# Optimization experiments

Measured on AMD Instinct MI355X. Metric: run time of the kernel, lower is better.

Reference implementation:

```python
import jax, jax.numpy as jnp
import numpy as np

N_HEADS = 16
HEAD_DIM = 64
ROPE_BASE = 10000.0


def _rope_cos_sin(T, d, dtype):
    # GPT-NeoX style: inv_freq over even indices, cos/sin duplicated to full head_dim
    inv_freq = 1.0 / (ROPE_BASE ** (jnp.arange(0, d, 2, dtype=jnp.float32) / d))
    freqs = jnp.arange(T, dtype=jnp.float32)[:, None] * inv_freq[None, :]  # [T, d/2]
    emb = jnp.concatenate([freqs, freqs], axis=-1)  # [T, d]
    return jnp.cos(emb).astype(dtype), jnp.sin(emb).astype(dtype)


def _rotate_half(x):
    x1, x2 = jnp.split(x, 2, axis=-1)
    return jnp.concatenate([-x2, x1], axis=-1)


def setup_inputs() -> dict:
    key = jax.random.key(0)
    k1, k2, k3 = jax.random.split(key, 3)
    B, T, C = 2, 2048, 1024
    x = jax.random.normal(k1, (B, T, C), dtype=jnp.float32)
    Wqkv = jax.random.normal(k2, (C, 3 * C), dtype=jnp.float32) * (1.0 / np.sqrt(C))
    Wout = jax.random.normal(k3, (C, C), dtype=jnp.float32) * (1.0 / np.sqrt(C))
    return {"x": x, "Wqkv": Wqkv, "Wout": Wout}


def reference(x, Wqkv, Wout):
    B, T, C = x.shape
    H, D = N_HEADS, HEAD_DIM
    qkv = (x @ Wqkv).reshape(B, T, 3, H, D)
    q, k, v = qkv[:, :, 0], qkv[:, :, 1], qkv[:, :, 2]  # [B,T,H,D]
    q = q.transpose(0, 2, 1, 3)  # [B,H,T,D]
    k = k.transpose(0, 2, 1, 3)
    v = v.transpose(0, 2, 1, 3)
    cos, sin = _rope_cos_sin(T, D, x.dtype)  # [T,D]
    cos = cos[None, None]
    sin = sin[None, None]
    q = q * cos + _rotate_half(q) * sin
    k = k * cos + _rotate_half(k) * sin
    scale = 1.0 / np.sqrt(D)
    scores = jnp.einsum("bhqd,bhkd->bhqk", q, k) * scale  # [B,H,T,T]
    causal = jnp.tril(jnp.ones((T, T), dtype=bool))
    scores = jnp.where(causal[None, None], scores, jnp.finfo(scores.dtype).min)
    attn = jax.nn.softmax(scores, axis=-1)
    out = jnp.einsum("bhqk,bhkd->bhqd", attn, v)  # [B,H,T,D]
    out = out.transpose(0, 2, 1, 3).reshape(B, T, C)
    return out @ Wout
```

## Files before the change

kernel.cpp:

```cpp
#include <hip/hip_runtime.h>


#define B_  2
#define T_  2048
#define C_  1024
#define H_  16
#define D_  64
#define N3_ 3072

typedef unsigned short ushortx8 __attribute__((ext_vector_type(8)));
typedef unsigned short ushortx4 __attribute__((ext_vector_type(4)));
typedef short bf16x8 __attribute__((ext_vector_type(8)));
typedef float f32x4 __attribute__((ext_vector_type(4)));
typedef float f32x16 __attribute__((ext_vector_type(16)));
typedef unsigned int uintx2 __attribute__((ext_vector_type(2)));

__device__ __forceinline__ unsigned short f2bf(float f) {
  union { float f; unsigned u; } v; v.f = f;
  unsigned r = v.u + 0x7FFFu + ((v.u >> 16) & 1u);
  return (unsigned short)(r >> 16);
}
__device__ __forceinline__ float bf2f(unsigned short h) {
  union { unsigned u; float f; } v; v.u = ((unsigned)h) << 16;
  return v.f;
}
__device__ __forceinline__ unsigned cvtpk_bf16(float lo, float hi) {
  unsigned r; asm("v_cvt_pk_bf16_f32 %0, %1, %2" : "=v"(r) : "v"(lo), "v"(hi));
  return r;
}
__device__ __forceinline__ void gload_lds16(const void* g, void* l) {
  __builtin_amdgcn_global_load_lds((const __attribute__((address_space(1))) void*)g,
                                   (__attribute__((address_space(3))) void*)l,
                                   16, 0, 0);
}

__global__ __launch_bounds__(256) void prep_kernel(const float* __restrict__ x,
                                                   unsigned short* __restrict__ Xb,
                                                   const float* __restrict__ Wqkv,
                                                   unsigned short* __restrict__ WqkvT,
                                                   const float* __restrict__ Wout,
                                                   unsigned short* __restrict__ WoutT) {
  __shared__ float tile[32][33];
  const int bid = blockIdx.x;
  if (bid < 4096) {
    size_t i = ((size_t)bid * 256 + threadIdx.x) * 4;
    const float4 v = *(const float4*)(x + i);
    ushortx4 o;
    o[0] = f2bf(v.x); o[1] = f2bf(v.y); o[2] = f2bf(v.z); o[3] = f2bf(v.w);
    *(ushortx4*)(Xb + i) = o;
    return;
  }
  const float* W;
  unsigned short* WT;
  int K, N, n0, k0;
  if (bid < 7168) {
    const int idx = bid - 4096;
    W = Wqkv; WT = WqkvT; K = C_; N = N3_;
    n0 = (idx % (N3_ / 32)) * 32; k0 = (idx / (N3_ / 32)) * 32;
  } else {
    const int idx = bid - 7168;
    W = Wout; WT = WoutT; K = C_; N = C_;
    n0 = (idx % (C_ / 32)) * 32; k0 = (idx / (C_ / 32)) * 32;
  }
  const int tx = threadIdx.x & 31, ty = threadIdx.x >> 5;
#pragma unroll
  for (int i = 0; i < 4; ++i)
    tile[ty + i * 8][tx] = W[(size_t)(k0 + ty + i * 8) * N + n0 + tx];
  __syncthreads();
#pragma unroll
  for (int i = 0; i < 4; ++i)
    WT[(size_t)(n0 + ty + i * 8) * K + k0 + tx] = f2bf(tile[tx][ty + i * 8]);
}

template <int OUTF32>
__global__ __launch_bounds__(256) void gemm_bt_kernel(const unsigned short* __restrict__ A,
                                                      const unsigned short* __restrict__ BT,
                                                      void* __restrict__ Cptr,
                                                      int M, int N, int K) {
  __shared__ unsigned short Alds[128 * 64];
  __shared__ unsigned short Blds[128 * 64];
  const int tid = threadIdx.x;
  const int w = tid >> 6, l = tid & 63;
  const int wr = w >> 1, wc = w & 1;
  const int lg = l >> 4, lr = l & 15;
  const int m0 = blockIdx.y * 128, n0 = blockIdx.x * 128;
  const int lr8 = l >> 3;
  const int lc8 = (l & 7) ^ lr8;

  f32x4 acc[4][4];
#pragma unroll
  for (int i = 0; i < 4; ++i)
#pragma unroll
    for (int j = 0; j < 4; ++j) acc[i][j] = f32x4{0.f, 0.f, 0.f, 0.f};

  for (int k0 = 0; k0 < K; k0 += 64) {
    __syncthreads();
#pragma unroll
    for (int i = 0; i < 4; ++i) {
      const int ch = w * 4 + i;
      gload_lds16(A + (size_t)(m0 + ch * 8 + lr8) * K + k0 + lc8 * 8, &Alds[ch * 512]);
      gload_lds16(BT + (size_t)(n0 + ch * 8 + lr8) * K + k0 + lc8 * 8, &Blds[ch * 512]);
    }
    __syncthreads();
#pragma unroll
    for (int kc = 0; kc < 2; ++kc) {
      bf16x8 af[4], bfr[4];
#pragma unroll
      for (int mi = 0; mi < 4; ++mi) {
        const int row = wr * 64 + mi * 16 + lr;
        const int c16 = (kc * 4 + lg) ^ (row & 7);
        af[mi] = *(const bf16x8*)(&Alds[row * 64 + c16 * 8]);
      }
#pragma unroll
      for (int nj = 0; nj < 4; ++nj) {
        const int row = wc * 64 + nj * 16 + lr;
        const int c16 = (kc * 4 + lg) ^ (row & 7);
        bfr[nj] = *(const bf16x8*)(&Blds[row * 64 + c16 * 8]);
      }
#pragma unroll
      for (int mi = 0; mi < 4; ++mi)
#pragma unroll
        for (int nj = 0; nj < 4; ++nj)
          acc[mi][nj] = __builtin_amdgcn_mfma_f32_16x16x32_bf16(af[mi], bfr[nj], acc[mi][nj], 0, 0, 0);
    }
  }
#pragma unroll
  for (int mi = 0; mi < 4; ++mi)
#pragma unroll
    for (int nj = 0; nj < 4; ++nj)
#pragma unroll
      for (int j = 0; j < 4; ++j) {
        const int row = m0 + wr * 64 + mi * 16 + lg * 4 + j;
        const int col = n0 + wc * 64 + nj * 16 + lr;
        if (OUTF32) ((float*)Cptr)[(size_t)row * N + col] = acc[mi][nj][j];
        else ((unsigned short*)Cptr)[(size_t)row * N + col] = f2bf(acc[mi][nj][j]);
      }
}

__global__ __launch_bounds__(256) void rope_vtrans_kernel(const unsigned short* __restrict__ QKV,
                                                          unsigned short* __restrict__ Qp,
                                                          unsigned short* __restrict__ Kp,
                                                          unsigned short* __restrict__ Vt) {
  __shared__ unsigned short tile[64][72];
  const int tt = blockIdx.x, bh = blockIdx.y;
  const int b = bh >> 4, h = bh & 15;
  const int tid = threadIdx.x;
  if (blockIdx.z == 0) {
    const int half = tid >> 7;
    const int r = (tid >> 1) & 63;
    const int d0 = (tid & 1) * 16;
    const int t = tt * 64 + r;
    const unsigned short* src = QKV + (size_t)(b * T_ + t) * N3_ + half * C_ + h * D_;
    ushortx8 lo0 = *(const ushortx8*)(src + d0);
    ushortx8 lo1 = *(const ushortx8*)(src + d0 + 8);
    ushortx8 hi0 = *(const ushortx8*)(src + d0 + 32);
    ushortx8 hi1 = *(const ushortx8*)(src + d0 + 40);
    ushortx8 olo0, olo1, ohi0, ohi1;
    const float scale = half ? 1.0f : 0.18033688011112042f;
    const float tf = (float)t;
#pragma unroll
    for (int jj = 0; jj < 16; ++jj) {
      const int d = d0 + jj;
      const float invf = exp2f((float)d * -0.41524101186092036f);
      const float ang = tf * invf;
      const float c = cosf(ang), s = sinf(ang);
      const float xl = bf2f(jj < 8 ? lo0[jj] : lo1[jj - 8]);
      const float xh = bf2f(jj < 8 ? hi0[jj] : hi1[jj - 8]);
      const unsigned short rl = f2bf((xl * c - xh * s) * scale);
      const unsigned short rh = f2bf((xh * c + xl * s) * scale);
      if (jj < 8) { olo0[jj] = rl; ohi0[jj] = rh; }
      else        { olo1[jj - 8] = rl; ohi1[jj - 8] = rh; }
    }
    unsigned short* dst = (half ? Kp : Qp) + ((size_t)bh * T_ + t) * D_;
    *(ushortx8*)(dst + d0) = olo0;
    *(ushortx8*)(dst + d0 + 8) = olo1;
    *(ushortx8*)(dst + d0 + 32) = ohi0;
    *(ushortx8*)(dst + d0 + 40) = ohi1;
  } else {
    {
      const int r = tid >> 2, seg = tid & 3;
      const unsigned short* src = QKV + (size_t)(b * T_ + tt * 64 + r) * N3_ + 2 * C_ + h * D_ + seg * 16;
      *(ushortx8*)(&tile[r][seg * 16]) = *(const ushortx8*)(src);
      *(ushortx8*)(&tile[r][seg * 16 + 8]) = *(const ushortx8*)(src + 8);
    }
    __syncthreads();
    {
      const int d = tid >> 2, ts = tid & 3;
      ushortx8 o0, o1;
#pragma unroll
      for (int i = 0; i < 8; ++i) { o0[i] = tile[ts * 16 + i][d]; o1[i] = tile[ts * 16 + 8 + i][d]; }
      unsigned short* dst = Vt + ((size_t)bh * D_ + d) * T_ + tt * 64 + ts * 16;
      *(ushortx8*)(dst) = o0;
      *(ushortx8*)(dst + 8) = o1;
    }
  }
}

__global__ __launch_bounds__(256, 2) void attn7_kernel(const unsigned short* __restrict__ Qp,
                                                       const unsigned short* __restrict__ Kp,
                                                       const unsigned short* __restrict__ Vt,
                                                       unsigned short* __restrict__ Ob) {
  __shared__ unsigned short Klds[3][64 * 64];
  __shared__ unsigned short Vlds[3][64 * 64];
  const int tid = threadIdx.x, w = tid >> 6, l = tid & 63;
  const int lq = l & 31, hi = l >> 5;
  const int swz = lq & 7;
  const int bid = blockIdx.x;
  const int bh = bid & 31;
  const int pp = bid >> 5;
  const int p = (pp < 8) ? pp : 23 - pp;
  const int s = (w < 2) ? (2 * p + w) : (62 - 2 * p + (w - 2));
  const int q0 = s * 32;
  const int ntiles = 32 - p;
  const size_t koff = (size_t)bh * T_ * D_;
  const unsigned short* Kb = Kp + koff;
  const unsigned short* Vb = Vt + (size_t)bh * D_ * T_;

  const int lr8 = l >> 3;
  const int lc8 = (l & 7) ^ lr8;

  bf16x8 qf[4];
  {
    const unsigned short* qp = Qp + koff + (size_t)(q0 + lq) * D_ + hi * 8;
#pragma unroll
    for (int ds = 0; ds < 4; ++ds) qf[ds] = *(const bf16x8*)(qp + ds * 16);
  }
  f32x16 o0, o1;
#pragma unroll
  for (int r = 0; r < 16; ++r) { o0[r] = 0.f; o1[r] = 0.f; }
  float m = -3.0e38f, lden = 0.f;

#pragma unroll
  for (int i = 0; i < 2; ++i) {
    const int c = w * 2 + i;
    gload_lds16(Kb + (size_t)(c * 8 + lr8) * D_ + lc8 * 8, &Klds[0][c * 512]);
    gload_lds16(Vb + (size_t)(c * 8 + lr8) * T_ + lc8 * 8, &Vlds[0][c * 512]);
  }

  for (int kt = 0; kt < ntiles; ++kt) {
    const int cur = kt % 3;
    const int nxt = (kt + 1) % 3;
    const int ktn = (kt + 1 < ntiles) ? kt + 1 : kt;
    const int kvn = ktn * 64;
#pragma unroll
    for (int i = 0; i < 2; ++i) {
      const int c = w * 2 + i;
      gload_lds16(Kb + (size_t)(kvn + c * 8 + lr8) * D_ + lc8 * 8, &Klds[nxt][c * 512]);
      gload_lds16(Vb + (size_t)(c * 8 + lr8) * T_ + kvn + lc8 * 8, &Vlds[nxt][c * 512]);
    }
    asm volatile("s_waitcnt vmcnt(4)" ::: "memory");
    __builtin_amdgcn_s_barrier();
    __builtin_amdgcn_sched_barrier(0);

    const int kv0 = kt * 64;
    if (kv0 <= q0 + 31) {
      const unsigned short* KL = &Klds[cur][0];
      const unsigned short* VL = &Vlds[cur][0];
      f32x16 acc0, acc1;
#pragma unroll
      for (int r = 0; r < 16; ++r) { acc0[r] = 0.f; acc1[r] = 0.f; }
      __builtin_amdgcn_s_setprio(1);
#pragma unroll
      for (int ds = 0; ds < 4; ++ds) {
        const int slot = ((ds * 2 + hi) ^ swz) * 8;
        const bf16x8 kf0 = *(const bf16x8*)(&KL[(lq) * 64 + slot]);
        const bf16x8 kf1 = *(const bf16x8*)(&KL[(32 + lq) * 64 + slot]);
        acc0 = __builtin_amdgcn_mfma_f32_32x32x16_bf16(kf0, qf[ds], acc0, 0, 0, 0);
        acc1 = __builtin_amdgcn_mfma_f32_32x32x16_bf16(kf1, qf[ds], acc1, 0, 0, 0);
      }
      __builtin_amdgcn_s_setprio(0);
      if (kv0 + 63 > q0) {
        const int thr0 = q0 + lq - kv0;
        const int thr1 = thr0 - 32;
#pragma unroll
        for (int r = 0; r < 16; ++r) {
          const int kvloc = (r & 3) + 8 * (r >> 2) + 4 * hi;
          if (kvloc > thr0) acc0[r] = -3.0e38f;
          if (kvloc > thr1) acc1[r] = -3.0e38f;
        }
      }
      float mx[8];
#pragma unroll
      for (int i = 0; i < 8; ++i)
        mx[i] = fmaxf(fmaxf(acc0[i], acc0[i + 8]), fmaxf(acc1[i], acc1[i + 8]));
#pragma unroll
      for (int i = 0; i < 4; ++i) mx[i] = fmaxf(mx[i], mx[i + 4]);
      const float mloc = fmaxf(fmaxf(mx[0], mx[1]), fmaxf(mx[2], mx[3]));
      const uintx2 mp = __builtin_amdgcn_permlane32_swap(__float_as_uint(mloc), __float_as_uint(mloc), false, false);
      const float pm = fmaxf(__uint_as_float(mp.x), __uint_as_float(mp.y));
      const bool grow = pm > m + 8.0f;
      if (__any(grow)) {
        const float mn = grow ? pm : m;
        const float alpha = __builtin_amdgcn_exp2f(m - mn);
        m = mn;
        lden *= alpha;
#pragma unroll
        for (int r = 0; r < 16; ++r) { o0[r] *= alpha; o1[r] *= alpha; }
      }
      float p0[16], p1[16];
#pragma unroll
      for (int r = 0; r < 16; ++r) {
        p0[r] = __builtin_amdgcn_exp2f(acc0[r] - m);
        p1[r] = __builtin_amdgcn_exp2f(acc1[r] - m);
      }
      unsigned W0 = cvtpk_bf16(p0[0], p0[1]), W1 = cvtpk_bf16(p0[2], p0[3]);
      unsigned W2 = cvtpk_bf16(p0[4], p0[5]), W3 = cvtpk_bf16(p0[6], p0[7]);
      uintx2 Aa = __builtin_amdgcn_permlane32_swap(W0, W2, false, false);
      uintx2 Ab = __builtin_amdgcn_permlane32_swap(W1, W3, false, false);
      union { unsigned u[4]; bf16x8 v; } pfa0 = {{Aa.x, Ab.x, Aa.y, Ab.y}};
      W0 = cvtpk_bf16(p0[8], p0[9]);   W1 = cvtpk_bf16(p0[10], p0[11]);
      W2 = cvtpk_bf16(p0[12], p0[13]); W3 = cvtpk_bf16(p0[14], p0[15]);
      Aa = __builtin_amdgcn_permlane32_swap(W0, W2, false, false);
      Ab = __builtin_amdgcn_permlane32_swap(W1, W3, false, false);
      union { unsigned u[4]; bf16x8 v; } pfa1 = {{Aa.x, Ab.x, Aa.y, Ab.y}};
      W0 = cvtpk_bf16(p1[0], p1[1]);   W1 = cvtpk_bf16(p1[2], p1[3]);
      W2 = cvtpk_bf16(p1[4], p1[5]);   W3 = cvtpk_bf16(p1[6], p1[7]);
      Aa = __builtin_amdgcn_permlane32_swap(W0, W2, false, false);
      Ab = __builtin_amdgcn_permlane32_swap(W1, W3, false, false);
      union { unsigned u[4]; bf16x8 v; } pfb0 = {{Aa.x, Ab.x, Aa.y, Ab.y}};
      W0 = cvtpk_bf16(p1[8], p1[9]);   W1 = cvtpk_bf16(p1[10], p1[11]);
      W2 = cvtpk_bf16(p1[12], p1[13]); W3 = cvtpk_bf16(p1[14], p1[15]);
      Aa = __builtin_amdgcn_permlane32_swap(W0, W2, false, false);
      Ab = __builtin_amdgcn_permlane32_swap(W1, W3, false, false);
      union { unsigned u[4]; bf16x8 v; } pfb1 = {{Aa.x, Ab.x, Aa.y, Ab.y}};

      __builtin_amdgcn_s_setprio(1);
#pragma unroll
      for (int dt = 0; dt < 2; ++dt) {
        const int rowb = (dt * 32 + lq) * 64;
        const bf16x8 vf0 = *(const bf16x8*)(&VL[rowb + ((0 * 2 + hi) ^ swz) * 8]);
        const bf16x8 vf1 = *(const bf16x8*)(&VL[rowb + ((1 * 2 + hi) ^ swz) * 8]);
        const bf16x8 vf2 = *(const bf16x8*)(&VL[rowb + ((2 * 2 + hi) ^ swz) * 8]);
        const bf16x8 vf3 = *(const bf16x8*)(&VL[rowb + ((3 * 2 + hi) ^ swz) * 8]);
        if (dt == 0) {
          o0 = __builtin_amdgcn_mfma_f32_32x32x16_bf16(vf0, pfa0.v, o0, 0, 0, 0);
          o0 = __builtin_amdgcn_mfma_f32_32x32x16_bf16(vf1, pfa1.v, o0, 0, 0, 0);
          o0 = __builtin_amdgcn_mfma_f32_32x32x16_bf16(vf2, pfb0.v, o0, 0, 0, 0);
          o0 = __builtin_amdgcn_mfma_f32_32x32x16_bf16(vf3, pfb1.v, o0, 0, 0, 0);
        } else {
          o1 = __builtin_amdgcn_mfma_f32_32x32x16_bf16(vf0, pfa0.v, o1, 0, 0, 0);
          o1 = __builtin_amdgcn_mfma_f32_32x32x16_bf16(vf1, pfa1.v, o1, 0, 0, 0);
          o1 = __builtin_amdgcn_mfma_f32_32x32x16_bf16(vf2, pfb0.v, o1, 0, 0, 0);
          o1 = __builtin_amdgcn_mfma_f32_32x32x16_bf16(vf3, pfb1.v, o1, 0, 0, 0);
        }
      }
      __builtin_amdgcn_s_setprio(0);
      float sm[8];
#pragma unroll
      for (int i = 0; i < 8; ++i) sm[i] = (p0[i] + p0[i + 8]) + (p1[i] + p1[i + 8]);
#pragma unroll
      for (int i = 0; i < 4; ++i) sm[i] = sm[i] + sm[i + 4];
      const float sloc = (sm[0] + sm[1]) + (sm[2] + sm[3]);
      const uintx2 sp = __builtin_amdgcn_permlane32_swap(__float_as_uint(sloc), __float_as_uint(sloc), false, false);
      lden += __uint_as_float(sp.x) + __uint_as_float(sp.y);
    }
  }
  asm volatile("s_waitcnt vmcnt(0)" ::: "memory");

  const float rl = __builtin_amdgcn_rcpf(lden);
  const int b = bh >> 4, hh = bh & 15;
  unsigned short* orow = Ob + (size_t)(b * T_ + q0 + lq) * C_ + hh * D_ + 4 * hi;
#pragma unroll
  for (int rq = 0; rq < 4; ++rq) {
    ushortx4 ov0, ov1;
#pragma unroll
    for (int i = 0; i < 4; ++i) {
      ov0[i] = f2bf(o0[rq * 4 + i] * rl);
      ov1[i] = f2bf(o1[rq * 4 + i] * rl);
    }
    *(ushortx4*)(orow + rq * 8) = ov0;
    *(ushortx4*)(orow + 32 + rq * 8) = ov1;
  }
}

extern "C" void kernel_launch(void* const* d_in, const int* in_sizes, int n_in,
                              void* d_out, int out_size, void* d_ws, size_t ws_size,
                              hipStream_t stream) {
  const float* x = (const float*)d_in[0];
  const float* Wqkv = (const float*)d_in[1];
  const float* Wout = (const float*)d_in[2];
  float* out = (float*)d_out;
  char* ws = (char*)d_ws;
  unsigned short* Xb    = (unsigned short*)(ws);
  unsigned short* WqkvT = (unsigned short*)(ws + (8ull << 20));
  unsigned short* WoutT = (unsigned short*)(ws + (14ull << 20));
  unsigned short* QKVb  = (unsigned short*)(ws + (16ull << 20));
  unsigned short* Qp    = (unsigned short*)(ws + (40ull << 20));
  unsigned short* Kp    = (unsigned short*)(ws + (48ull << 20));
  unsigned short* Vt    = (unsigned short*)(ws + (56ull << 20));
  unsigned short* Ob    = (unsigned short*)(ws + (64ull << 20));

  prep_kernel<<<8192, 256, 0, stream>>>(x, Xb, Wqkv, WqkvT, Wout, WoutT);
  gemm_bt_kernel<0><<<dim3(N3_ / 128, (B_ * T_) / 128), 256, 0, stream>>>(
      Xb, WqkvT, QKVb, B_ * T_, N3_, C_);
  rope_vtrans_kernel<<<dim3(T_ / 64, B_ * H_, 2), 256, 0, stream>>>(QKVb, Qp, Kp, Vt);
  attn7_kernel<<<512, 256, 0, stream>>>(Qp, Kp, Vt, Ob);
  gemm_bt_kernel<1><<<dim3(C_ / 128, (B_ * T_) / 128), 256, 0, stream>>>(
      Ob, WoutT, out, B_ * T_, C_, C_);
}
```

Before: 119.0 us.

## Split KV tiles across waves per 64-row query block and merge partial softmax

```diff
diff --git a/kernel.cpp b/kernel.cpp
--- a/kernel.cpp
+++ b/kernel.cpp
@@ -196,134 +196,194 @@
   }
 }
 
-__global__ __launch_bounds__(256, 2) void attn7_kernel(const unsigned short* __restrict__ Qp,
+__global__ __launch_bounds__(256, 2) void attn8_kernel(const unsigned short* __restrict__ Qp,
                                                        const unsigned short* __restrict__ Kp,
                                                        const unsigned short* __restrict__ Vt,
                                                        unsigned short* __restrict__ Ob) {
-  __shared__ unsigned short Klds[3][64 * 64];
-  __shared__ unsigned short Vlds[3][64 * 64];
+  __shared__ unsigned short shm[24576];
+  __shared__ float mstat[2][2][4][32];
   const int tid = threadIdx.x, w = tid >> 6, l = tid & 63;
   const int lq = l & 31, hi = l >> 5;
   const int swz = lq & 7;
   const int bid = blockIdx.x;
   const int bh = bid & 31;
-  const int pp = bid >> 5;
-  const int p = (pp < 8) ? pp : 23 - pp;
-  const int s = (w < 2) ? (2 * p + w) : (62 - 2 * p + (w - 2));
-  const int q0 = s * 32;
-  const int ntiles = 32 - p;
+  const int j = bid >> 5;
+  const int r = j & 7, q2 = j >> 3;
+  const int g = (q2 == 0) ? (31 - r) : (q2 == 1) ? (16 + r) : (q2 == 2) ? (15 - r) : r;
+  const int q0 = g * 64;
+  const int ntiles = g + 1;
   const size_t koff = (size_t)bh * T_ * D_;
   const unsigned short* Kb = Kp + koff;
   const unsigned short* Vb = Vt + (size_t)bh * D_ * T_;
-
-  const int lr8 = l >> 3;
-  const int lc8 = (l & 7) ^ lr8;
-
-  bf16x8 qf[4];
+  const int lr8 = l >> 3, lc8 = (l & 7) ^ lr8;
+
+  bf16x8 qlo[4], qhi[4];
   {
     const unsigned short* qp = Qp + koff + (size_t)(q0 + lq) * D_ + hi * 8;
 #pragma unroll
-    for (int ds = 0; ds < 4; ++ds) qf[ds] = *(const bf16x8*)(qp + ds * 16);
-  }
-  f32x16 o0, o1;
-#pragma unroll
-  for (int r = 0; r < 16; ++r) { o0[r] = 0.f; o1[r] = 0.f; }
-  float m = -3.0e38f, lden = 0.f;
+    for (int ds = 0; ds < 4; ++ds) {
+      qlo[ds] = *(const bf16x8*)(qp + ds * 16);
+      qhi[ds] = *(const bf16x8*)(qp + 32 * D_ + ds * 16);
+    }
+  }
+  f32x16 oA0, oA1, oB0, oB1;
+#pragma unroll
+  for (int i = 0; i < 16; ++i) { oA0[i] = 0.f; oA1[i] = 0.f; oB0[i] = 0.f; oB1[i] = 0.f; }
+  float mA = -3.0e38f, lA = 0.f, mB = -3.0e38f, lB = 0.f;
 
 #pragma unroll
   for (int i = 0; i < 2; ++i) {
     const int c = w * 2 + i;
-    gload_lds16(Kb + (size_t)(c * 8 + lr8) * D_ + lc8 * 8, &Klds[0][c * 512]);
-    gload_lds16(Vb + (size_t)(c * 8 + lr8) * T_ + lc8 * 8, &Vlds[0][c * 512]);
+    gload_lds16(Kb + (size_t)(c * 8 + lr8) * D_ + lc8 * 8, &shm[c * 512]);
+    gload_lds16(Vb + (size_t)(c * 8 + lr8) * T_ + lc8 * 8, &shm[12288 + c * 512]);
   }
 
   for (int kt = 0; kt < ntiles; ++kt) {
-    const int cur = kt % 3;
-    const int nxt = (kt + 1) % 3;
+    const int cur = kt % 3, nxt = (kt + 1) % 3;
     const int ktn = (kt + 1 < ntiles) ? kt + 1 : kt;
     const int kvn = ktn * 64;
 #pragma unroll
     for (int i = 0; i < 2; ++i) {
       const int c = w * 2 + i;
-      gload_lds16(Kb + (size_t)(kvn + c * 8 + lr8) * D_ + lc8 * 8, &Klds[nxt][c * 512]);
-      gload_lds16(Vb + (size_t)(c * 8 + lr8) * T_ + kvn + lc8 * 8, &Vlds[nxt][c * 512]);
+      gload_lds16(Kb + (size_t)(kvn + c * 8 + lr8) * D_ + lc8 * 8, &shm[nxt * 4096 + c * 512]);
+      gload_lds16(Vb + (size_t)(c * 8 + lr8) * T_ + kvn + lc8 * 8, &shm[12288 + nxt * 4096 + c * 512]);
     }
     asm volatile("s_waitcnt vmcnt(4)" ::: "memory");
     __builtin_amdgcn_s_barrier();
     __builtin_amdgcn_sched_barrier(0);
 
-    const int kv0 = kt * 64;
-    if (kv0 <= q0 + 31) {
-      const unsigned short* KL = &Klds[cur][0];
-      const unsigned short* VL = &Vlds[cur][0];
-      f32x16 acc0, acc1;
-#pragma unroll
-      for (int r = 0; r < 16; ++r) { acc0[r] = 0.f; acc1[r] = 0.f; }
+    if ((kt & 3) == w) {
+      const unsigned short* KL = &shm[cur * 4096];
+      const unsigned short* VL = &shm[12288 + cur * 4096];
+      f32x16 aL0, aL1, aH0, aH1;
+#pragma unroll
+      for (int i = 0; i < 16; ++i) { aL0[i] = 0.f; aL1[i] = 0.f; aH0[i] = 0.f; aH1[i] = 0.f; }
       __builtin_amdgcn_s_setprio(1);
 #pragma unroll
       for (int ds = 0; ds < 4; ++ds) {
         const int slot = ((ds * 2 + hi) ^ swz) * 8;
-        const bf16x8 kf0 = *(const bf16x8*)(&KL[(lq) * 64 + slot]);
+        const bf16x8 kf0 = *(const bf16x8*)(&KL[lq * 64 + slot]);
         const bf16x8 kf1 = *(const bf16x8*)(&KL[(32 + lq) * 64 + slot]);
-        acc0 = __builtin_amdgcn_mfma_f32_32x32x16_bf16(kf0, qf[ds], acc0, 0, 0, 0);
-        acc1 = __builtin_amdgcn_mfma_f32_32x32x16_bf16(kf1, qf[ds], acc1, 0, 0, 0);
+        aL0 = __builtin_amdgcn_mfma_f32_32x32x16_bf16(kf0, qlo[ds], aL0, 0, 0, 0);
+        aL1 = __builtin_amdgcn_mfma_f32_32x32x16_bf16(kf1, qlo[ds], aL1, 0, 0, 0);
+        aH0 = __builtin_amdgcn_mfma_f32_32x32x16_bf16(kf0, qhi[ds], aH0, 0, 0, 0);
+        aH1 = __builtin_amdgcn_mfma_f32_32x32x16_bf16(kf1, qhi[ds], aH1, 0, 0, 0);
       }
       __builtin_amdgcn_s_setprio(0);
-      if (kv0 + 63 > q0) {
-        const int thr0 = q0 + lq - kv0;
-        const int thr1 = thr0 - 32;
-#pragma unroll
-        for (int r = 0; r < 16; ++r) {
-          const int kvloc = (r & 3) + 8 * (r >> 2) + 4 * hi;
-          if (kvloc > thr0) acc0[r] = -3.0e38f;
-          if (kvloc > thr1) acc1[r] = -3.0e38f;
+      if (kt == g) {
+#pragma unroll
+        for (int rr = 0; rr < 16; ++rr) {
+          const int kvloc = (rr & 3) + 8 * (rr >> 2) + 4 * hi;
+          if (kvloc > lq) { aL0[rr] = -3.0e38f; aH1[rr] = -3.0e38f; }
+          aL1[rr] = -3.0e38f;
         }
       }
-      float mx[8];
-#pragma unroll
-      for (int i = 0; i < 8; ++i)
-        mx[i] = fmaxf(fmaxf(acc0[i], acc0[i + 8]), fmaxf(acc1[i], acc1[i + 8]));
-#pragma unroll
-      for (int i = 0; i < 4; ++i) mx[i] = fmaxf(mx[i], mx[i + 4]);
-      const float mloc = fmaxf(fmaxf(mx[0], mx[1]), fmaxf(mx[2], mx[3]));
-      const uintx2 mp = __builtin_amdgcn_permlane32_swap(__float_as_uint(mloc), __float_as_uint(mloc), false, false);
-      const float pm = fmaxf(__uint_as_float(mp.x), __uint_as_float(mp.y));
-      const bool grow = pm > m + 8.0f;
-      if (__any(grow)) {
-        const float mn = grow ? pm : m;
-        const float alpha = __builtin_amdgcn_exp2f(m - mn);
-        m = mn;
-        lden *= alpha;
-#pragma unroll
-        for (int r = 0; r < 16; ++r) { o0[r] *= alpha; o1[r] *= alpha; }
-      }
       float p0[16], p1[16];
-#pragma unroll
-      for (int r = 0; r < 16; ++r) {
-        p0[r] = __builtin_amdgcn_exp2f(acc0[r] - m);
-        p1[r] = __builtin_amdgcn_exp2f(acc1[r] - m);
-      }
-      unsigned W0 = cvtpk_bf16(p0[0], p0[1]), W1 = cvtpk_bf16(p0[2], p0[3]);
-      unsigned W2 = cvtpk_bf16(p0[4], p0[5]), W3 = cvtpk_bf16(p0[6], p0[7]);
-      uintx2 Aa = __builtin_amdgcn_permlane32_swap(W0, W2, false, false);
-      uintx2 Ab = __builtin_amdgcn_permlane32_swap(W1, W3, false, false);
-      union { unsigned u[4]; bf16x8 v; } pfa0 = {{Aa.x, Ab.x, Aa.y, Ab.y}};
-      W0 = cvtpk_bf16(p0[8], p0[9]);   W1 = cvtpk_bf16(p0[10], p0[11]);
-      W2 = cvtpk_bf16(p0[12], p0[13]); W3 = cvtpk_bf16(p0[14], p0[15]);
-      Aa = __builtin_amdgcn_permlane32_swap(W0, W2, false, false);
-      Ab = __builtin_amdgcn_permlane32_swap(W1, W3, false, false);
-      union { unsigned u[4]; bf16x8 v; } pfa1 = {{Aa.x, Ab.x, Aa.y, Ab.y}};
-      W0 = cvtpk_bf16(p1[0], p1[1]);   W1 = cvtpk_bf16(p1[2], p1[3]);
-      W2 = cvtpk_bf16(p1[4], p1[5]);   W3 = cvtpk_bf16(p1[6], p1[7]);
-      Aa = __builtin_amdgcn_permlane32_swap(W0, W2, false, false);
-      Ab = __builtin_amdgcn_permlane32_swap(W1, W3, false, false);
-      union { unsigned u[4]; bf16x8 v; } pfb0 = {{Aa.x, Ab.x, Aa.y, Ab.y}};
-      W0 = cvtpk_bf16(p1[8], p1[9]);   W1 = cvtpk_bf16(p1[10], p1[11]);
-      W2 = cvtpk_bf16(p1[12], p1[13]); W3 = cvtpk_bf16(p1[14], p1[15]);
-      Aa = __builtin_amdgcn_permlane32_swap(W0, W2, false, false);
-      Ab = __builtin_amdgcn_permlane32_swap(W1, W3, false, false);
-      union { unsigned u[4]; bf16x8 v; } pfb1 = {{Aa.x, Ab.x, Aa.y, Ab.y}};
-
+      bf16x8 pfL0, pfL1, pfL2, pfL3, pfH0, pfH1, pfH2, pfH3;
+      {
+        float mx[8];
+#pragma unroll
+        for (int i = 0; i < 8; ++i)
+          mx[i] = fmaxf(fmaxf(aL0[i], aL0[i + 8]), fmaxf(aL1[i], aL1[i + 8]));
+#pragma unroll
+        for (int i = 0; i < 4; ++i) mx[i] = fmaxf(mx[i], mx[i + 4]);
+        const float mloc = fmaxf(fmaxf(mx[0], mx[1]), fmaxf(mx[2], mx[3]));
+        const uintx2 mp = __builtin_amdgcn_permlane32_swap(__float_as_uint(mloc), __float_as_uint(mloc), false, false);
+        const float pm = fmaxf(__uint_as_float(mp.x), __uint_as_float(mp.y));
+        const bool grow = pm > mA + 8.0f;
+        if (__any(grow)) {
+          const float mn = grow ? pm : mA;
+          const float alpha = __builtin_amdgcn_exp2f(mA - mn);
+          mA = mn; lA *= alpha;
+#pragma unroll
+          for (int i = 0; i < 16; ++i) { oA0[i] *= alpha; oA1[i] *= alpha; }
+        }
+#pragma unroll
+        for (int i = 0; i < 16; ++i) {
+          p0[i] = __builtin_amdgcn_exp2f(aL0[i] - mA);
+          p1[i] = __builtin_amdgcn_exp2f(aL1[i] - mA);
+        }
+        unsigned W0 = cvtpk_bf16(p0[0], p0[1]), W1 = cvtpk_bf16(p0[2], p0[3]);
+        unsigned W2 = cvtpk_bf16(p0[4], p0[5]), W3 = cvtpk_bf16(p0[6], p0[7]);
+        uintx2 Aa = __builtin_amdgcn_permlane32_swap(W0, W2, false, false);
+        uintx2 Ab = __builtin_amdgcn_permlane32_swap(W1, W3, false, false);
+        { union { unsigned u[4]; bf16x8 v; } t = {{Aa.x, Ab.x, Aa.y, Ab.y}}; pfL0 = t.v; }
+        W0 = cvtpk_bf16(p0[8], p0[9]);   W1 = cvtpk_bf16(p0[10], p0[11]);
+        W2 = cvtpk_bf16(p0[12], p0[13]); W3 = cvtpk_bf16(p0[14], p0[15]);
+        Aa = __builtin_amdgcn_permlane32_swap(W0, W2, false, false);
+        Ab = __builtin_amdgcn_permlane32_swap(W1, W3, false, false);
+        { union { unsigned u[4]; bf16x8 v; } t = {{Aa.x, Ab.x, Aa.y, Ab.y}}; pfL1 = t.v; }
+        W0 = cvtpk_bf16(p1[0], p1[1]);   W1 = cvtpk_bf16(p1[2], p1[3]);
+        W2 = cvtpk_bf16(p1[4], p1[5]);   W3 = cvtpk_bf16(p1[6], p1[7]);
+        Aa = __builtin_amdgcn_permlane32_swap(W0, W2, false, false);
+        Ab = __builtin_amdgcn_permlane32_swap(W1, W3, false, false);
+        { union { unsigned u[4]; bf16x8 v; } t = {{Aa.x, Ab.x, Aa.y, Ab.y}}; pfL2 = t.v; }
+        W0 = cvtpk_bf16(p1[8], p1[9]);   W1 = cvtpk_bf16(p1[10], p1[11]);
+        W2 = cvtpk_bf16(p1[12], p1[13]); W3 = cvtpk_bf16(p1[14], p1[15]);
+        Aa = __builtin_amdgcn_permlane32_swap(W0, W2, false, false);
+        Ab = __builtin_amdgcn_permlane32_swap(W1, W3, false, false);
+        { union { unsigned u[4]; bf16x8 v; } t = {{Aa.x, Ab.x, Aa.y, Ab.y}}; pfL3 = t.v; }
+        float sm[8];
+#pragma unroll
+        for (int i = 0; i < 8; ++i) sm[i] = (p0[i] + p0[i + 8]) + (p1[i] + p1[i + 8]);
+#pragma unroll
+        for (int i = 0; i < 4; ++i) sm[i] = sm[i] + sm[i + 4];
+        const float sloc = (sm[0] + sm[1]) + (sm[2] + sm[3]);
+        const uintx2 sp = __builtin_amdgcn_permlane32_swap(__float_as_uint(sloc), __float_as_uint(sloc), false, false);
+        lA += __uint_as_float(sp.x) + __uint_as_float(sp.y);
+      }
+      {
+        float mx[8];
+#pragma unroll
+        for (int i = 0; i < 8; ++i)
+          mx[i] = fmaxf(fmaxf(aH0[i], aH0[i + 8]), fmaxf(aH1[i], aH1[i + 8]));
+#pragma unroll
+        for (int i = 0; i < 4; ++i) mx[i] = fmaxf(mx[i], mx[i + 4]);
+        const float mloc = fmaxf(fmaxf(mx[0], mx[1]), fmaxf(mx[2], mx[3]));
+        const uintx2 mp = __builtin_amdgcn_permlane32_swap(__float_as_uint(mloc), __float_as_uint(mloc), false, false);
+        const float pm = fmaxf(__uint_as_float(mp.x), __uint_as_float(mp.y));
+        const bool grow = pm > mB + 8.0f;
+        if (__any(grow)) {
+          const float mn = grow ? pm : mB;
+          const float alpha = __builtin_amdgcn_exp2f(mB - mn);
+          mB = mn; lB *= alpha;
+#pragma unroll
+          for (int i = 0; i < 16; ++i) { oB0[i] *= alpha; oB1[i] *= alpha; }
+        }
+#pragma unroll
+        for (int i = 0; i < 16; ++i) {
+          p0[i] = __builtin_amdgcn_exp2f(aH0[i] - mB);
+          p1[i] = __builtin_amdgcn_exp2f(aH1[i] - mB);
+        }
+        unsigned W0 = cvtpk_bf16(p0[0], p0[1]), W1 = cvtpk_bf16(p0[2], p0[3]);
+        unsigned W2 = cvtpk_bf16(p0[4], p0[5]), W3 = cvtpk_bf16(p0[6], p0[7]);
+        uintx2 Aa = __builtin_amdgcn_permlane32_swap(W0, W2, false, false);
+        uintx2 Ab = __builtin_amdgcn_permlane32_swap(W1, W3, false, false);
+        { union { unsigned u[4]; bf16x8 v; } t = {{Aa.x, Ab.x, Aa.y, Ab.y}}; pfH0 = t.v; }
+        W0 = cvtpk_bf16(p0[8], p0[9]);   W1 = cvtpk_bf16(p0[10], p0[11]);
+        W2 = cvtpk_bf16(p0[12], p0[13]); W3 = cvtpk_bf16(p0[14], p0[15]);
+        Aa = __builtin_amdgcn_permlane32_swap(W0, W2, false, false);
+        Ab = __builtin_amdgcn_permlane32_swap(W1, W3, false, false);
+        { union { unsigned u[4]; bf16x8 v; } t = {{Aa.x, Ab.x, Aa.y, Ab.y}}; pfH1 = t.v; }
+        W0 = cvtpk_bf16(p1[0], p1[1]);   W1 = cvtpk_bf16(p1[2], p1[3]);
+        W2 = cvtpk_bf16(p1[4], p1[5]);   W3 = cvtpk_bf16(p1[6], p1[7]);
+        Aa = __builtin_amdgcn_permlane32_swap(W0, W2, false, false);
+        Ab = __builtin_amdgcn_permlane32_swap(W1, W3, false, false);
+        { union { unsigned u[4]; bf16x8 v; } t = {{Aa.x, Ab.x, Aa.y, Ab.y}}; pfH2 = t.v; }
+        W0 = cvtpk_bf16(p1[8], p1[9]);   W1 = cvtpk_bf16(p1[10], p1[11]);
+        W2 = cvtpk_bf16(p1[12], p1[13]); W3 = cvtpk_bf16(p1[14], p1[15]);
+        Aa = __builtin_amdgcn_permlane32_swap(W0, W2, false, false);
+        Ab = __builtin_amdgcn_permlane32_swap(W1, W3, false, false);
+        { union { unsigned u[4]; bf16x8 v; } t = {{Aa.x, Ab.x, Aa.y, Ab.y}}; pfH3 = t.v; }
+        float sm[8];
+#pragma unroll
+        for (int i = 0; i < 8; ++i) sm[i] = (p0[i] + p0[i + 8]) + (p1[i] + p1[i + 8]);
+#pragma unroll
+        for (int i = 0; i < 4; ++i) sm[i] = sm[i] + sm[i + 4];
+        const float sloc = (sm[0] + sm[1]) + (sm[2] + sm[3]);
+        const uintx2 sp = __builtin_amdgcn_permlane32_swap(__float_as_uint(sloc), __float_as_uint(sloc), false, false);
+        lB += __uint_as_float(sp.x) + __uint_as_float(sp.y);
+      }
       __builtin_amdgcn_s_setprio(1);
 #pragma unroll
       for (int dt = 0; dt < 2; ++dt) {
@@ -333,43 +393,85 @@
         const bf16x8 vf2 = *(const bf16x8*)(&VL[rowb + ((2 * 2 + hi) ^ swz) * 8]);
         const bf16x8 vf3 = *(const bf16x8*)(&VL[rowb + ((3 * 2 + hi) ^ swz) * 8]);
         if (dt == 0) {
-          o0 = __builtin_amdgcn_mfma_f32_32x32x16_bf16(vf0, pfa0.v, o0, 0, 0, 0);
-          o0 = __builtin_amdgcn_mfma_f32_32x32x16_bf16(vf1, pfa1.v, o0, 0, 0, 0);
-          o0 = __builtin_amdgcn_mfma_f32_32x32x16_bf16(vf2, pfb0.v, o0, 0, 0, 0);
-          o0 = __builtin_amdgcn_mfma_f32_32x32x16_bf16(vf3, pfb1.v, o0, 0, 0, 0);
+          oA0 = __builtin_amdgcn_mfma_f32_32x32x16_bf16(vf0, pfL0, oA0, 0, 0, 0);
+          oA0 = __builtin_amdgcn_mfma_f32_32x32x16_bf16(vf1, pfL1, oA0, 0, 0, 0);
+          oA0 = __builtin_amdgcn_mfma_f32_32x32x16_bf16(vf2, pfL2, oA0, 0, 0, 0);
+          oA0 = __builtin_amdgcn_mfma_f32_32x32x16_bf16(vf3, pfL3, oA0, 0, 0, 0);
+          oB0 = __builtin_amdgcn_mfma_f32_32x32x16_bf16(vf0, pfH0, oB0, 0, 0, 0);
+          oB0 = __builtin_amdgcn_mfma_f32_32x32x16_bf16(vf1, pfH1, oB0, 0, 0, 0);
+          oB0 = __builtin_amdgcn_mfma_f32_32x32x16_bf16(vf2, pfH2, oB0, 0, 0, 0);
+          oB0 = __builtin_amdgcn_mfma_f32_32x32x16_bf16(vf3, pfH3, oB0, 0, 0, 0);
         } else {
-          o1 = __builtin_amdgcn_mfma_f32_32x32x16_bf16(vf0, pfa0.v, o1, 0, 0, 0);
-          o1 = __builtin_amdgcn_mfma_f32_32x32x16_bf16(vf1, pfa1.v, o1, 0, 0, 0);
-          o1 = __builtin_amdgcn_mfma_f32_32x32x16_bf16(vf2, pfb0.v, o1, 0, 0, 0);
-          o1 = __builtin_amdgcn_mfma_f32_32x32x16_bf16(vf3, pfb1.v, o1, 0, 0, 0);
+          oA1 = __builtin_amdgcn_mfma_f32_32x32x16_bf16(vf0, pfL0, oA1, 0, 0, 0);
+          oA1 = __builtin_amdgcn_mfma_f32_32x32x16_bf16(vf1, pfL1, oA1, 0, 0, 0);
+          oA1 = __builtin_amdgcn_mfma_f32_32x32x16_bf16(vf2, pfL2, oA1, 0, 0, 0);
+          oA1 = __builtin_amdgcn_mfma_f32_32x32x16_bf16(vf3, pfL3, oA1, 0, 0, 0);
+          oB1 = __builtin_amdgcn_mfma_f32_32x32x16_bf16(vf0, pfH0, oB1, 0, 0, 0);
+          oB1 = __builtin_amdgcn_mfma_f32_32x32x16_bf16(vf1, pfH1, oB1, 0, 0, 0);
+          oB1 = __builtin_amdgcn_mfma_f32_32x32x16_bf16(vf2, pfH2, oB1, 0, 0, 0);
+          oB1 = __builtin_amdgcn_mfma_f32_32x32x16_bf16(vf3, pfH3, oB1, 0, 0, 0);
         }
       }
       __builtin_amdgcn_s_setprio(0);
-      float sm[8];
-#pragma unroll
-      for (int i = 0; i < 8; ++i) sm[i] = (p0[i] + p0[i + 8]) + (p1[i] + p1[i + 8]);
-#pragma unroll
-      for (int i = 0; i < 4; ++i) sm[i] = sm[i] + sm[i + 4];
-      const float sloc = (sm[0] + sm[1]) + (sm[2] + sm[3]);
-      const uintx2 sp = __builtin_amdgcn_permlane32_swap(__float_as_uint(sloc), __float_as_uint(sloc), false, false);
-      lden += __uint_as_float(sp.x) + __uint_as_float(sp.y);
     }
   }
   asm volatile("s_waitcnt vmcnt(0)" ::: "memory");
-
-  const float rl = __builtin_amdgcn_rcpf(lden);
+  __builtin_amdgcn_s_barrier();
+
+  {
+#pragma unroll
+    for (int s2 = 0; s2 < 2; ++s2) {
+      unsigned short* prow = &shm[((s2 * 4 + w) * 64 + l) * 36];
+      ushortx4 t0;
+#pragma unroll
+      for (int s4 = 0; s4 < 4; ++s4) {
+#pragma unroll
+        for (int i = 0; i < 4; ++i) t0[i] = f2bf(s2 ? oB0[s4 * 4 + i] : oA0[s4 * 4 + i]);
+        *(ushortx4*)(prow + s4 * 4) = t0;
+      }
+#pragma unroll
+      for (int s4 = 0; s4 < 4; ++s4) {
+#pragma unroll
+        for (int i = 0; i < 4; ++i) t0[i] = f2bf(s2 ? oB1[s4 * 4 + i] : oA1[s4 * 4 + i]);
+        *(ushortx4*)(prow + 16 + s4 * 4) = t0;
+      }
+    }
+    if (hi == 0) {
+      mstat[0][0][w][lq] = mA; mstat[0][1][w][lq] = lA;
+      mstat[1][0][w][lq] = mB; mstat[1][1][w][lq] = lB;
+    }
+  }
+  __syncthreads();
+
   const int b = bh >> 4, hh = bh & 15;
-  unsigned short* orow = Ob + (size_t)(b * T_ + q0 + lq) * C_ + hh * D_ + 4 * hi;
-#pragma unroll
-  for (int rq = 0; rq < 4; ++rq) {
+#pragma unroll
+  for (int s2 = 0; s2 < 2; ++s2) {
+    float mw[4], lw[4];
+#pragma unroll
+    for (int w2 = 0; w2 < 4; ++w2) { mw[w2] = mstat[s2][0][w2][lq]; lw[w2] = mstat[s2][1][w2][lq]; }
+    const float M = fmaxf(fmaxf(mw[0], mw[1]), fmaxf(mw[2], mw[3]));
+    float fw[4], L = 0.f;
+#pragma unroll
+    for (int w2 = 0; w2 < 4; ++w2) { fw[w2] = __builtin_amdgcn_exp2f(mw[w2] - M); L += lw[w2] * fw[w2]; }
+    float a0[4] = {0.f, 0.f, 0.f, 0.f}, a1[4] = {0.f, 0.f, 0.f, 0.f};
+#pragma unroll
+    for (int w2 = 0; w2 < 4; ++w2) {
+      const unsigned short* prow = &shm[((s2 * 4 + w2) * 64 + l) * 36];
+      const ushortx4 pa = *(const ushortx4*)(prow + w * 4);
+      const ushortx4 pb = *(const ushortx4*)(prow + 16 + w * 4);
+#pragma unroll
+      for (int i = 0; i < 4; ++i) {
+        a0[i] += fw[w2] * bf2f(pa[i]);
+        a1[i] += fw[w2] * bf2f(pb[i]);
+      }
+    }
+    const float rl = __builtin_amdgcn_rcpf(L);
+    unsigned short* orow = Ob + (size_t)(b * T_ + q0 + s2 * 32 + lq) * C_ + hh * D_ + 4 * hi;
     ushortx4 ov0, ov1;
 #pragma unroll
-    for (int i = 0; i < 4; ++i) {
-      ov0[i] = f2bf(o0[rq * 4 + i] * rl);
-      ov1[i] = f2bf(o1[rq * 4 + i] * rl);
-    }
-    *(ushortx4*)(orow + rq * 8) = ov0;
-    *(ushortx4*)(orow + 32 + rq * 8) = ov1;
+    for (int i = 0; i < 4; ++i) { ov0[i] = f2bf(a0[i] * rl); ov1[i] = f2bf(a1[i] * rl); }
+    *(ushortx4*)(orow + w * 8) = ov0;
+    *(ushortx4*)(orow + 32 + w * 8) = ov1;
   }
 }
 
@@ -394,7 +496,7 @@
   gemm_bt_kernel<0><<<dim3(N3_ / 128, (B_ * T_) / 128), 256, 0, stream>>>(
       Xb, WqkvT, QKVb, B_ * T_, N3_, C_);
   rope_vtrans_kernel<<<dim3(T_ / 64, B_ * H_, 2), 256, 0, stream>>>(QKVb, Qp, Kp, Vt);
-  attn7_kernel<<<512, 256, 0, stream>>>(Qp, Kp, Vt, Ob);
+  attn8_kernel<<<1024, 256, 0, stream>>>(Qp, Kp, Vt, Ob);
   gemm_bt_kernel<1><<<dim3(C_ / 128, (B_ * T_) / 128), 256, 0, stream>>>(
       Ob, WoutT, out, B_ * T_, C_, C_);
 }
```

Measured after the change: 149.1 us. 25.4% more time.
